# Kernel optimization log

Hardware: AMD Instinct MI355X
Metric: run time of the kernel (lower is better)

The kernel has to match this reference:

```python
import jax, jax.numpy as jnp
import numpy as np

ROWS, COLS, H, W = 128, 128, 128, 128
B, C = 2, 16
DENSITY = 0.01  # classic Hough vote matrix is very sparse binary


def setup_inputs() -> dict:
    key = jax.random.key(0)
    k_img, k_vote = jax.random.split(key)
    image = jax.random.normal(k_img, (B, C, ROWS, COLS), dtype=jnp.float32)
    # sparse binary voting matrix, shape (rows, cols, h, w)
    vote_index = (jax.random.uniform(k_vote, (ROWS, COLS, H, W)) < DENSITY).astype(jnp.float32)
    return {"image": image, "vote_index": vote_index}


def reference(image, vote_index):
    rows, cols, h, w = vote_index.shape
    b, c = image.shape[0], image.shape[1]
    V = vote_index.reshape(rows * cols, h * w)          # (rows*cols, h*w)
    x = jax.nn.relu(image.reshape(b * c, rows * cols))  # (b*c, rows*cols)
    ht = (x @ V) / cols                                 # (b*c, h*w)
    return ht.reshape(b, c, h, w)
```

## Files before the change

kernel.cpp:

```cpp
#include <hip/hip_runtime.h>

constexpr int Mdim = 32;
constexpr int Kdim = 16384;
constexpr int Ndim = 16384;

constexpr int TPB  = 256;
constexpr int GTPB = 512;

constexpr int BN     = 512;
constexpr int NB     = Ndim / BN;
constexpr int KT     = 16;
constexpr int KC     = Kdim / KT;
constexpr int NSTAGE = KC / 16;

typedef short bf16x8 __attribute__((ext_vector_type(8)));
typedef float f32x16 __attribute__((ext_vector_type(16)));

__device__ __forceinline__ short f32_to_bf16(float f) {
    union { float f; unsigned u; } c; c.f = f;
    unsigned u = c.u;
    u += 0x7fffu + ((u >> 16) & 1u);
    return (short)(u >> 16);
}

__global__ __launch_bounds__(TPB)
void build_xa(const float* __restrict__ image, short* __restrict__ xa) {
    const int g    = blockIdx.x * TPB + threadIdx.x;
    const int lane = g & 63;
    const int slab = g >> 6;
    const int m    = lane & 31;
    const int k    = slab * 16 + (lane >> 5) * 8;
    const float* src = image + (size_t)m * Kdim + k;

    bf16x8 o;
    #pragma unroll
    for (int j = 0; j < 8; ++j)
        o[j] = f32_to_bf16(fmaxf(src[j], 0.0f) * (1.0f / 128.0f));
    reinterpret_cast<bf16x8*>(xa)[g] = o;
}

__device__ __forceinline__ void glds16(const float* src, float* dst) {
    __builtin_amdgcn_global_load_lds(
        (const __attribute__((address_space(1))) void*)src,
        (__attribute__((address_space(3))) void*)dst,
        16, 0, 0);
}

__global__ __launch_bounds__(GTPB, 4)
void ht_gemm(const short* __restrict__ xa,
             const float* __restrict__ vote,
             float* __restrict__ parts)
{
    __shared__ float vbuf[2][16 * BN];

    const int tid  = threadIdx.x;
    const int lane = tid & 63;
    const int w    = tid >> 6;
    const int nb   = blockIdx.x & (NB - 1);
    const int kch  = blockIdx.x >> 5;
    const int k0   = kch * KC;
    const int n0   = nb * BN;

    const int nlo  = lane & 31;
    const int krow = (lane >> 5) * 8;
    const int r0   = 2 * w;

    const short* abase = xa + ((size_t)(k0 / 16) * 64 + lane) * 8;

    f32x16 acc0, acc1;
    #pragma unroll
    for (int i = 0; i < 16; ++i) { acc0[i] = 0.0f; acc1[i] = 0.0f; }

    auto stage = [&](int buf, int s) {
        const float* rp = vote + (size_t)(k0 + s * 16 + r0) * Ndim + n0;
        #pragma unroll
        for (int i = 0; i < 4; ++i) {
            const float* src = rp + (size_t)(i >> 1) * Ndim + (i & 1) * 256 + lane * 4;
            glds16(src, &vbuf[buf][(r0 + (i >> 1)) * BN + (i & 1) * 256]);
        }
    };

    stage(0, 0);
    bf16x8 aC = *reinterpret_cast<const bf16x8*>(abase);

    int cur = 0;
    for (int s = 0; s < NSTAGE; ++s) {
        bf16x8 aN = aC;
        if (s + 1 < NSTAGE) {
            stage(cur ^ 1, s + 1);
            aN = *reinterpret_cast<const bf16x8*>(abase + (size_t)(s + 1) * 512);
            asm volatile("s_waitcnt vmcnt(5)" ::: "memory");
        } else {
            asm volatile("s_waitcnt vmcnt(0)" ::: "memory");
        }
        __builtin_amdgcn_s_barrier();
        asm volatile("" ::: "memory");

        const float* vb = &vbuf[cur][krow * BN + w * 64 + nlo];
        bf16x8 b0, b1;
        #pragma unroll
        for (int j = 0; j < 8; ++j) {
            union { float f; unsigned u; } c0, c1;
            c0.f = vb[j * BN];
            c1.f = vb[j * BN + 32];
            b0[j] = (short)(c0.u >> 16);
            b1[j] = (short)(c1.u >> 16);
        }
        acc0 = __builtin_amdgcn_mfma_f32_32x32x16_bf16(aC, b0, acc0, 0, 0, 0);
        acc1 = __builtin_amdgcn_mfma_f32_32x32x16_bf16(aC, b1, acc1, 0, 0, 0);

        __builtin_amdgcn_s_barrier();
        asm volatile("" ::: "memory");
        aC = aN; cur ^= 1;
    }

    float* pb = parts + (size_t)kch * ((size_t)Mdim * Ndim);
    const int c0    = n0 + w * 64 + nlo;
    const int rbase = 4 * (lane >> 5);
    #pragma unroll
    for (int r = 0; r < 16; ++r) {
        const int row = (r & 3) + 8 * (r >> 2) + rbase;
        pb[(size_t)row * Ndim + c0]      = acc0[r];
        pb[(size_t)row * Ndim + c0 + 32] = acc1[r];
    }
}

__global__ __launch_bounds__(TPB)
void ht_reduce(const float* __restrict__ parts, float* __restrict__ out, int nchunks) {
    const size_t i4 = (size_t)blockIdx.x * TPB + threadIdx.x;
    const float4* p = reinterpret_cast<const float4*>(parts) + i4;
    float4 s = make_float4(0.f, 0.f, 0.f, 0.f);
    constexpr size_t stride4 = (size_t)Mdim * Ndim / 4;
    for (int c = 0; c < nchunks; ++c) {
        const float4 v = p[(size_t)c * stride4];
        s.x += v.x; s.y += v.y; s.z += v.z; s.w += v.w;
    }
    reinterpret_cast<float4*>(out)[i4] = s;
}

__global__ __launch_bounds__(TPB)
void ht_gemm_atomic(const float* __restrict__ image, const float* __restrict__ vote,
                    float* __restrict__ out) {
    __shared__ float xsh[256 * Mdim];
    const int tid = threadIdx.x;
    const int ntile = blockIdx.x % 16;
    const int k0 = (blockIdx.x / 16) * 256;
    const int nn0 = ntile * 1024 + tid * 4;
    for (int idx = tid; idx < 256 * Mdim; idx += TPB) {
        const int kk = idx >> 5, m = idx & 31;
        xsh[idx] = fmaxf(image[(size_t)m * Kdim + (k0 + kk)], 0.0f) * (1.0f / 128.0f);
    }
    __syncthreads();
    float4 acc[Mdim];
    #pragma unroll
    for (int m = 0; m < Mdim; ++m) acc[m] = make_float4(0.f, 0.f, 0.f, 0.f);
    const float* vptr = vote + (size_t)k0 * Ndim + nn0;
    for (int kk = 0; kk < 256; ++kk) {
        const float4 v = *reinterpret_cast<const float4*>(vptr);
        vptr += Ndim;
        #pragma unroll
        for (int m = 0; m < Mdim; ++m) {
            const float s = xsh[kk * Mdim + m];
            acc[m].x = fmaf(s, v.x, acc[m].x); acc[m].y = fmaf(s, v.y, acc[m].y);
            acc[m].z = fmaf(s, v.z, acc[m].z); acc[m].w = fmaf(s, v.w, acc[m].w);
        }
    }
    #pragma unroll
    for (int m = 0; m < Mdim; ++m) {
        float* o = out + (size_t)m * Ndim + nn0;
        unsafeAtomicAdd(o + 0, acc[m].x); unsafeAtomicAdd(o + 1, acc[m].y);
        unsafeAtomicAdd(o + 2, acc[m].z); unsafeAtomicAdd(o + 3, acc[m].w);
    }
}

extern "C" void kernel_launch(void* const* d_in, const int* in_sizes, int n_in,
                              void* d_out, int out_size, void* d_ws, size_t ws_size,
                              hipStream_t stream) {
    const float* image = (const float*)d_in[0];
    const float* vote  = (const float*)d_in[1];
    float* out = (float*)d_out;

    const size_t xa_bytes    = (size_t)(Kdim / 16) * 64 * 8 * sizeof(short);
    const size_t chunk_bytes = (size_t)Mdim * Ndim * sizeof(float);

    if (xa_bytes + (size_t)KT * chunk_bytes > ws_size) {
        (void)hipMemsetAsync(out, 0, (size_t)out_size * sizeof(float), stream);
        ht_gemm_atomic<<<dim3(16 * 64), TPB, 0, stream>>>(image, vote, out);
        return;
    }

    short* xa    = (short*)d_ws;
    float* parts = (float*)((char*)d_ws + xa_bytes);

    build_xa<<<dim3((Kdim / 16) * 64 / TPB), TPB, 0, stream>>>(image, xa);
    ht_gemm<<<dim3(NB * KT), GTPB, 0, stream>>>(xa, vote, parts);
    ht_reduce<<<dim3((Mdim * Ndim) / (4 * TPB)), TPB, 0, stream>>>(parts, out, KT);
}
```

Baseline: 1.323 ms.

## Deepen vote-matrix prefetch to four LDS buffers and halve N tile

Replaces the double-buffered LDS staging with a four-buffer ring that keeps two to three stages of vote rows in flight. The N tile shrinks from 512 to 256 columns and the K split drops from 16 to 8 chunks, so each wave runs one MFMA per stage instead of two. Grid size stays at 512 blocks, and the partial-sum buffer and reduce pass are half as large. The intent is to hide global-to-LDS latency on this memory-bound GEMM, at the cost of less compute per barrier and longer per-block K loops.

```diff
diff --git a/kernel.cpp b/kernel.cpp
--- a/kernel.cpp
+++ b/kernel.cpp
@@ -7,9 +7,9 @@
 constexpr int TPB  = 256;
 constexpr int GTPB = 512;
 
-constexpr int BN     = 512;
+constexpr int BN     = 256;
 constexpr int NB     = Ndim / BN;
-constexpr int KT     = 16;
+constexpr int KT     = 8;
 constexpr int KC     = Kdim / KT;
 constexpr int NSTAGE = KC / 16;
 
@@ -46,18 +46,23 @@
         16, 0, 0);
 }
 
+#define BARRIER() do { asm volatile("" ::: "memory"); \
+                       __builtin_amdgcn_s_barrier();  \
+                       asm volatile("" ::: "memory"); } while (0)
+#define WAITV(n) asm volatile("s_waitcnt vmcnt(" #n ")" ::: "memory")
+
 __global__ __launch_bounds__(GTPB, 4)
 void ht_gemm(const short* __restrict__ xa,
              const float* __restrict__ vote,
              float* __restrict__ parts)
 {
-    __shared__ float vbuf[2][16 * BN];
+    __shared__ float vbuf[4][16 * BN];
 
     const int tid  = threadIdx.x;
     const int lane = tid & 63;
     const int w    = tid >> 6;
     const int nb   = blockIdx.x & (NB - 1);
-    const int kch  = blockIdx.x >> 5;
+    const int kch  = blockIdx.x >> 6;
     const int k0   = kch * KC;
     const int n0   = nb * BN;
 
@@ -67,61 +72,50 @@
 
     const short* abase = xa + ((size_t)(k0 / 16) * 64 + lane) * 8;
 
-    f32x16 acc0, acc1;
+    f32x16 acc;
     #pragma unroll
-    for (int i = 0; i < 16; ++i) { acc0[i] = 0.0f; acc1[i] = 0.0f; }
+    for (int i = 0; i < 16; ++i) acc[i] = 0.0f;
 
-    auto stage = [&](int buf, int s) {
-        const float* rp = vote + (size_t)(k0 + s * 16 + r0) * Ndim + n0;
+    bf16x8 ar0, ar1, ar2, ar3;
+
+    auto issue = [&](int b, int s, bf16x8& ar) {
+        const float* rp = vote + (size_t)(k0 + s * 16 + r0) * Ndim + n0 + lane * 4;
+        glds16(rp,        &vbuf[b][(r0)     * BN]);
+        glds16(rp + Ndim, &vbuf[b][(r0 + 1) * BN]);
+        ar = *reinterpret_cast<const bf16x8*>(abase + (size_t)s * 512);
+    };
+    auto compute = [&](int b, bf16x8 ar) {
+        const float* vb = &vbuf[b][krow * BN + w * 32 + nlo];
+        bf16x8 bf;
         #pragma unroll
-        for (int i = 0; i < 4; ++i) {
-            const float* src = rp + (size_t)(i >> 1) * Ndim + (i & 1) * 256 + lane * 4;
-            glds16(src, &vbuf[buf][(r0 + (i >> 1)) * BN + (i & 1) * 256]);
+        for (int j = 0; j < 8; ++j) {
+            union { float f; unsigned u; } c; c.f = vb[j * BN];
+            bf[j] = (short)(c.u >> 16);
         }
+        acc = __builtin_amdgcn_mfma_f32_32x32x16_bf16(ar, bf, acc, 0, 0, 0);
     };
 
-    stage(0, 0);
-    bf16x8 aC = *reinterpret_cast<const bf16x8*>(abase);
+    issue(0, 0, ar0);
+    issue(1, 1, ar1);
 
-    int cur = 0;
-    for (int s = 0; s < NSTAGE; ++s) {
-        bf16x8 aN = aC;
-        if (s + 1 < NSTAGE) {
-            stage(cur ^ 1, s + 1);
-            aN = *reinterpret_cast<const bf16x8*>(abase + (size_t)(s + 1) * 512);
-            asm volatile("s_waitcnt vmcnt(5)" ::: "memory");
-        } else {
-            asm volatile("s_waitcnt vmcnt(0)" ::: "memory");
-        }
-        __builtin_amdgcn_s_barrier();
-        asm volatile("" ::: "memory");
-
-        const float* vb = &vbuf[cur][krow * BN + w * 64 + nlo];
-        bf16x8 b0, b1;
-        #pragma unroll
-        for (int j = 0; j < 8; ++j) {
-            union { float f; unsigned u; } c0, c1;
-            c0.f = vb[j * BN];
-            c1.f = vb[j * BN + 32];
-            b0[j] = (short)(c0.u >> 16);
-            b1[j] = (short)(c1.u >> 16);
-        }
-        acc0 = __builtin_amdgcn_mfma_f32_32x32x16_bf16(aC, b0, acc0, 0, 0, 0);
-        acc1 = __builtin_amdgcn_mfma_f32_32x32x16_bf16(aC, b1, acc1, 0, 0, 0);
-
-        __builtin_amdgcn_s_barrier();
-        asm volatile("" ::: "memory");
-        aC = aN; cur ^= 1;
+    for (int s0 = 0; s0 < NSTAGE - 4; s0 += 4) {
+        issue(2, s0 + 2, ar2); WAITV(6); BARRIER(); compute(0, ar0);
+        issue(3, s0 + 3, ar3); WAITV(6); BARRIER(); compute(1, ar1);
+        issue(0, s0 + 4, ar0); WAITV(6); BARRIER(); compute(2, ar2);
+        issue(1, s0 + 5, ar1); WAITV(6); BARRIER(); compute(3, ar3);
     }
+    issue(2, NSTAGE - 2, ar2); WAITV(6); BARRIER(); compute(0, ar0);
+    issue(3, NSTAGE - 1, ar3); WAITV(6); BARRIER(); compute(1, ar1);
+                 WAITV(3); BARRIER(); compute(2, ar2);
+                 WAITV(0); BARRIER(); compute(3, ar3);
 
     float* pb = parts + (size_t)kch * ((size_t)Mdim * Ndim);
-    const int c0    = n0 + w * 64 + nlo;
+    const int c0    = n0 + w * 32 + nlo;
     const int rbase = 4 * (lane >> 5);
     #pragma unroll
     for (int r = 0; r < 16; ++r) {
         const int row = (r & 3) + 8 * (r >> 2) + rbase;
-        pb[(size_t)row * Ndim + c0]      = acc0[r];
-        pb[(size_t)row * Ndim + c0 + 32] = acc1[r];
+        pb[(size_t)row * Ndim + c0] = acc[r];
     }
 }
 
```

Measured after the change: 1.310 ms. About the same (-1.0%).
